# Performance work log

Hardware: AMD Instinct MI355X
Metric: run time of the kernel (lower is better)

Reference implementation:

```python
import jax, jax.numpy as jnp
import numpy as np

N_NODES = 100000
N_EDGES = 1600000
IN_DIM = 128      # 1 (degree) + 127 (raw feat)
HID = 128
N_GRAPHS = 100


def setup_inputs() -> dict:
    key = jax.random.key(0)
    ks = jax.random.split(key, 16)
    feat = jax.random.normal(ks[0], (N_NODES, IN_DIM - 1), dtype=jnp.float32)
    src = jax.random.randint(ks[1], (N_EDGES,), 0, N_NODES, dtype=jnp.int32)
    dst = jax.random.randint(ks[2], (N_EDGES,), 0, N_NODES, dtype=jnp.int32)
    graph_ids = jnp.sort(jax.random.randint(ks[3], (N_NODES,), 0, N_GRAPHS, dtype=jnp.int32))
    s = 1.0 / np.sqrt(IN_DIM)
    W0 = jax.random.uniform(ks[4], (HID, IN_DIM), jnp.float32, -s, s)
    b0 = jax.random.uniform(ks[5], (HID,), jnp.float32, -s, s)
    s = 1.0 / np.sqrt(HID)
    W1 = jax.random.uniform(ks[6], (HID, HID), jnp.float32, -s, s)
    b1 = jax.random.uniform(ks[7], (HID,), jnp.float32, -s, s)
    W2 = jax.random.uniform(ks[8], (HID, HID), jnp.float32, -s, s)
    b2 = jax.random.uniform(ks[9], (HID,), jnp.float32, -s, s)
    Wc1 = jax.random.uniform(ks[10], (HID, HID), jnp.float32, -s, s)
    bc1 = jax.random.uniform(ks[11], (HID,), jnp.float32, -s, s)
    Wc2 = jax.random.uniform(ks[12], (1, HID), jnp.float32, -s, s)
    bc2 = jax.random.uniform(ks[13], (1,), jnp.float32, -s, s)
    return {"feat": feat, "src": src, "dst": dst, "graph_ids": graph_ids,
            "num_graphs": N_GRAPHS,
            "W0": W0, "b0": b0, "W1": W1, "b1": b1, "W2": W2, "b2": b2,
            "Wc1": Wc1, "bc1": bc1, "Wc2": Wc2, "bc2": bc2}


def _gcn_layer(h, src, dst, deg, W, b):
    # mean over in-neighbor messages; zero-in-degree nodes keep old h (DGL reduce never fires)
    n = h.shape[0]
    summed = jax.ops.segment_sum(h[src], dst, num_segments=n)  # [N, d]
    mean = summed / jnp.maximum(deg, 1.0)[:, None]
    agg = jnp.where((deg > 0)[:, None], mean, h)
    return jax.nn.relu(agg @ W.T + b)


def reference(feat, src, dst, graph_ids, num_graphs,
              W0, b0, W1, b1, W2, b2, Wc1, bc1, Wc2, bc2):
    n = feat.shape[0]
    deg = jax.ops.segment_sum(jnp.ones(src.shape[0], jnp.float32), dst, num_segments=n)  # in-degrees
    h = jnp.concatenate([deg[:, None], feat], axis=-1)  # [N, IN_DIM]
    for W, b in ((W0, b0), (W1, b1), (W2, b2)):
        h = _gcn_layer(h, src, dst, deg, W, b)
    # dgl.mean_nodes: per-graph mean of node features
    counts = jax.ops.segment_sum(jnp.ones(n, jnp.float32), graph_ids, num_segments=num_graphs)
    hg = jax.ops.segment_sum(h, graph_ids, num_segments=num_graphs) / jnp.maximum(counts, 1.0)[:, None]
    # faithful: classify1 applied twice, no activation (F.relu was passed as bias flag)
    hg = hg @ Wc1.T + bc1
    hg = hg @ Wc1.T + bc1
    hg = hg @ Wc2.T + bc2
    return hg  # [num_graphs, 1]
```

## Files before the change

kernel.cpp:

```cpp
#include <hip/hip_runtime.h>
#include <hip/hip_bf16.h>

#define HID 128
#define NRAW 127
#define BSH 8
#define BNODES 256
#define EW 1536


typedef __attribute__((ext_vector_type(8))) short short8;
typedef __attribute__((ext_vector_type(4))) float floatx4;
typedef __attribute__((ext_vector_type(2))) float floatx2;

__device__ inline unsigned pack_bf2(float x, float y) {
    unsigned bx = __float_as_uint(x);
    unsigned by = __float_as_uint(y);
    bx += 0x7fffu + ((bx >> 16) & 1u);
    by += 0x7fffu + ((by >> 16) & 1u);
    return (bx >> 16) | (by & 0xffff0000u);
}
__device__ inline float bf_lo(unsigned u) { return __uint_as_float(u << 16); }
__device__ inline float bf_hi(unsigned u) { return __uint_as_float(u & 0xffff0000u); }


__global__ void init_kernel(const float* __restrict__ W0, const float* __restrict__ W1,
                            const float* __restrict__ W2, const float* __restrict__ Wc1,
                            unsigned* __restrict__ O0, unsigned* __restrict__ O1,
                            unsigned* __restrict__ O2, float* __restrict__ Wc1p,
                            int* __restrict__ gbucket, float* __restrict__ hg,
                            float* __restrict__ counts, int G) {
    int id = blockIdx.x * blockDim.x + threadIdx.x;
    if (id < 512) gbucket[id] = 0;
    if (id < G * HID) hg[id] = 0.f;
    if (id < G) counts[id] = 0.f;
    if (id < 16384) {
        int t = id >> 7, p = id & 127;
        Wc1p[id] = Wc1[t * 128 + ((p & 7) * 16 + (p >> 3))];
    }
    if (id < 3 * 8192) {
        int sel = id >> 13, l = id & 8191;
        const float* W = sel == 0 ? W0 : (sel == 1 ? W1 : W2);
        unsigned* O = sel == 0 ? O0 : (sel == 1 ? O1 : O2);
        int o = l >> 6, pp = (l & 63) * 2;
        int k0 = (pp & 7) * 16 + (pp >> 3);
        int k1 = ((pp + 1) & 7) * 16 + ((pp + 1) >> 3);
        O[l] = pack_bf2(W[o * 128 + k0], W[o * 128 + k1]);
    }
}


__global__ __launch_bounds__(256) void bucket_count_kernel(const int* __restrict__ dst,
                                                           int* __restrict__ gbucket,
                                                           int E, int NB) {
    __shared__ int hist[512];
    int t = threadIdx.x;
    for (int b = t; b < NB; b += 256) hist[b] = 0;
    __syncthreads();
    int base = blockIdx.x * 4096;
    #pragma unroll
    for (int j = 0; j < 16; ++j) {
        int e = base + j * 256 + t;
        if (e < E) atomicAdd(&hist[dst[e] >> BSH], 1);
    }
    __syncthreads();
    for (int b = t; b < NB; b += 256) {
        int v = hist[b];
        if (v) atomicAdd(&gbucket[b], v);
    }
}

__global__ void bucket_scan_kernel(const int* __restrict__ gbucket, int* __restrict__ bstart,
                                   int* __restrict__ gcur, int NB, int E) {
    __shared__ int sm[512];
    int t = threadIdx.x;
    int v = (t < NB) ? gbucket[t] : 0;
    sm[t] = v;
    __syncthreads();
    for (int off = 1; off < 512; off <<= 1) {
        int add = (t >= off) ? sm[t - off] : 0;
        __syncthreads();
        sm[t] += add;
        __syncthreads();
    }
    if (t < NB) {
        int ex = sm[t] - v;
        bstart[t] = ex;
        gcur[t] = ex;
    }
    if (t == 0) bstart[NB] = E;
}

__global__ __launch_bounds__(256) void bucket_scatter_kernel(const int* __restrict__ src,
                                                             const int* __restrict__ dst,
                                                             int* __restrict__ gcur,
                                                             unsigned* __restrict__ staging,
                                                             int E, int NB) {
    __shared__ int hist[512];
    __shared__ int base[512];
    int t = threadIdx.x;
    for (int b = t; b < NB; b += 256) hist[b] = 0;
    __syncthreads();
    int s[16], d[16], r[16];
    int e0 = blockIdx.x * 4096;
    #pragma unroll
    for (int j = 0; j < 16; ++j) {
        int e = e0 + j * 256 + t;
        if (e < E) {
            s[j] = src[e];
            d[j] = dst[e];
            r[j] = atomicAdd(&hist[d[j] >> BSH], 1);
        } else d[j] = -1;
    }
    __syncthreads();
    for (int b = t; b < NB; b += 256) {
        int v = hist[b];
        base[b] = v ? atomicAdd(&gcur[b], v) : 0;
    }
    __syncthreads();
    #pragma unroll
    for (int j = 0; j < 16; ++j) {
        if (d[j] >= 0) {
            int b = d[j] >> BSH;
            staging[base[b] + r[j]] = ((unsigned)s[j] << 8) | ((unsigned)d[j] & 255u);
        }
    }
}

__global__ __launch_bounds__(256) void csr_build_kernel(const unsigned* __restrict__ staging,
                                                        const int* __restrict__ bstart,
                                                        int* __restrict__ rp, int* __restrict__ csr,
                                                        float* __restrict__ degf,
                                                        int N, int E, int NB) {
    __shared__ int hist[256];
    __shared__ int sm[256];
    __shared__ int excl[256];
    __shared__ int cnt[256];
    int t = threadIdx.x;
    int b = blockIdx.x;
    int nbase = b << BSH;
    int s0 = bstart[b], e1 = bstart[b + 1];
    hist[t] = 0;
    __syncthreads();
    for (int i = s0 + t; i < e1; i += 256) {
        unsigned p = staging[i];
        atomicAdd(&hist[p & (BNODES - 1)], 1);
    }
    __syncthreads();
    int h = hist[t];
    sm[t] = h;
    __syncthreads();
    for (int off = 1; off < 256; off <<= 1) {
        int add = (t >= off) ? sm[t - off] : 0;
        __syncthreads();
        sm[t] += add;
        __syncthreads();
    }
    excl[t] = sm[t] - h;
    cnt[t] = 0;
    int n = nbase + t;
    if (n < N) {
        rp[n] = s0 + (sm[t] - h);
        degf[n] = (float)h;
    }
    if (b == NB - 1 && t == 0) rp[N] = E;
    __syncthreads();
    for (int i = s0 + t; i < e1; i += 256) {
        unsigned p = staging[i];
        int dl = p & (BNODES - 1);
        int pos = s0 + excl[dl] + atomicAdd(&cnt[dl], 1);
        csr[pos] = (int)(p >> 8);
    }
}


__global__ void build_h0_kernel(const float* __restrict__ feat,
                                unsigned* __restrict__ h8, int N) {
    int id = blockIdx.x * blockDim.x + threadIdx.x;
    if (id >= N * 32) return;
    int n = id >> 5, c = id & 31;
    const float* fr = feat + (size_t)n * NRAW;
    int base = c >> 1, hb = (c & 1) * 4;
    float f[4];
    #pragma unroll
    for (int j = 0; j < 4; ++j) {
        int l = (hb + j) * 16 + base;
        f[j] = (l == 0) ? 0.f : fr[l - 1];
    }
    unsigned w = __builtin_amdgcn_cvt_pk_fp8_f32(f[0], f[1], 0, false);
    w = __builtin_amdgcn_cvt_pk_fp8_f32(f[2], f[3], w, true);
    h8[id] = w;
}


__global__ __launch_bounds__(256) void gcn_fused_kernel(const unsigned* __restrict__ h8,
                                                        unsigned* __restrict__ out8,
                                                        unsigned* __restrict__ outb,
                                                        const unsigned* __restrict__ Wb,
                                                        const float* __restrict__ bias,
                                                        const int* __restrict__ rp,
                                                        const int* __restrict__ csr,
                                                        const float* __restrict__ degf, int N) {
    __shared__ unsigned Al[16 * 64];
    __shared__ unsigned Cs[16 * 64];
    __shared__ int sIdx[EW];
    int t = threadIdx.x;
    int col = t & 15;
    int g = t >> 4;
    int n0 = blockIdx.x * 16;
    int i = n0 + g;
    const char* hbase = (const char*)h8;
    unsigned cOff = (unsigned)col * 8u;

    int start = 0, end = 0;
    if (i < N) { start = rp[i]; end = rp[i + 1]; }
    int deg = end - start;
    int nEnd = min(n0 + 16, N);
    int s0 = rp[n0];
    int e1 = rp[nEnd];

    floatx2 a0 = {0.f, 0.f}, a1 = {0.f, 0.f}, a2 = {0.f, 0.f}, a3 = {0.f, 0.f};
    float dsum = 0.f;

    #define GATH(ii) (*(const uint2*)(hbase + (((unsigned)(ii) << 7) + cOff)))
    #define ACC(vv) do { \
        a0 += __builtin_amdgcn_cvt_pk_f32_fp8((vv).x, false); \
        a1 += __builtin_amdgcn_cvt_pk_f32_fp8((vv).x, true);  \
        a2 += __builtin_amdgcn_cvt_pk_f32_fp8((vv).y, false); \
        a3 += __builtin_amdgcn_cvt_pk_f32_fp8((vv).y, true);  \
    } while (0)

    for (int w0 = s0; w0 < e1; w0 += EW) {
        if (w0 > s0) __syncthreads();
        int wcnt = min(EW, e1 - w0);
        for (int j = t; j < wcnt; j += 256) sIdx[j] = csr[w0 + j];
        __syncthreads();
        int p = max(start, w0) - w0;
        int pe = min(end, w0 + wcnt) - w0;
        for (; p + 8 <= pe; p += 8) {
            int i0 = sIdx[p],     i1 = sIdx[p + 1], i2 = sIdx[p + 2], i3 = sIdx[p + 3];
            int i4 = sIdx[p + 4], i5 = sIdx[p + 5], i6 = sIdx[p + 6], i7 = sIdx[p + 7];
            uint2 v0 = GATH(i0), v1 = GATH(i1), v2 = GATH(i2), v3 = GATH(i3);
            uint2 v4 = GATH(i4), v5 = GATH(i5), v6 = GATH(i6), v7 = GATH(i7);
            if (degf && col == 0)
                dsum += degf[i0] + degf[i1] + degf[i2] + degf[i3]
                      + degf[i4] + degf[i5] + degf[i6] + degf[i7];
            ACC(v0); ACC(v1); ACC(v2); ACC(v3);
            ACC(v4); ACC(v5); ACC(v6); ACC(v7);
        }
        for (; p + 4 <= pe; p += 4) {
            int i0 = sIdx[p], i1 = sIdx[p + 1], i2 = sIdx[p + 2], i3 = sIdx[p + 3];
            uint2 v0 = GATH(i0), v1 = GATH(i1), v2 = GATH(i2), v3 = GATH(i3);
            if (degf && col == 0)
                dsum += degf[i0] + degf[i1] + degf[i2] + degf[i3];
            ACC(v0); ACC(v1); ACC(v2); ACC(v3);
        }
        for (; p < pe; ++p) {
            int i0 = sIdx[p];
            uint2 v0 = GATH(i0);
            if (degf && col == 0) dsum += degf[i0];
            ACC(v0);
        }
    }

    if (i < N) {
        uint4 r;
        if (deg == 0) {
            uint2 v = GATH(i);
            floatx2 l0 = __builtin_amdgcn_cvt_pk_f32_fp8(v.x, false);
            floatx2 h0 = __builtin_amdgcn_cvt_pk_f32_fp8(v.x, true);
            floatx2 l1 = __builtin_amdgcn_cvt_pk_f32_fp8(v.y, false);
            floatx2 h1 = __builtin_amdgcn_cvt_pk_f32_fp8(v.y, true);
            r.x = pack_bf2(l0[0], l0[1]);
            r.y = pack_bf2(h0[0], h0[1]);
            r.z = pack_bf2(l1[0], l1[1]);
            r.w = pack_bf2(h1[0], h1[1]);
        } else {
            if (degf && col == 0) a0[0] = dsum;
            float inv = 1.f / (float)deg;
            r.x = pack_bf2(a0[0] * inv, a0[1] * inv);
            r.y = pack_bf2(a1[0] * inv, a1[1] * inv);
            r.z = pack_bf2(a2[0] * inv, a2[1] * inv);
            r.w = pack_bf2(a3[0] * inv, a3[1] * inv);
        }
        *(uint4*)&Al[(g * 16 + (col ^ (g & 7))) * 4] = r;
    }
    __syncthreads();

    int wv = t >> 6, lane = t & 63;
    int m = lane & 15, q = lane >> 4;
    floatx4 acc0 = (floatx4)(0.f), acc1 = (floatx4)(0.f);
    #pragma unroll
    for (int kt = 0; kt < 4; ++kt) {
        short8 af = *(const short8*)&Al[(m * 16 + ((kt * 4 + q) ^ (m & 7))) * 4];
        short8 b0 = *(const short8*)&Wb[((2 * wv) * 16 + m) * 64 + kt * 16 + q * 4];
        short8 b1 = *(const short8*)&Wb[((2 * wv + 1) * 16 + m) * 64 + kt * 16 + q * 4];
        acc0 = __builtin_amdgcn_mfma_f32_16x16x32_bf16(af, b0, acc0, 0, 0, 0);
        acc1 = __builtin_amdgcn_mfma_f32_16x16x32_bf16(af, b1, acc1, 0, 0, 0);
    }
    float bv0 = bias[(2 * wv) * 16 + m];
    float bv1 = bias[(2 * wv + 1) * 16 + m];
    #pragma unroll
    for (int r4 = 0; r4 < 4; ++r4) {
        int row = q * 4 + r4;
        float v0 = fmaxf(acc0[r4] + bv0, 0.f);
        float v1 = fmaxf(acc1[r4] + bv1, 0.f);
        if (out8) {
            unsigned pk = __builtin_amdgcn_cvt_pk_fp8_f32(v0, v1, 0, false);
            *(unsigned short*)((char*)Cs + row * 128 + m * 8 + 2 * wv) = (unsigned short)pk;
        } else {
            Cs[row * 64 + m * 4 + wv] = pack_bf2(v0, v1);
        }
    }
    __syncthreads();

    {
        int row = t >> 4, c = t & 15;
        int n = n0 + row;
        if (n < N) {
            if (out8)
                ((uint2*)out8)[(size_t)n * 16 + c] =
                    *(const uint2*)((const char*)Cs + row * 128 + c * 8);
            else
                ((uint4*)outb)[(size_t)n * 16 + c] = *(const uint4*)&Cs[row * 64 + c * 4];
        }
    }
    #undef GATH
    #undef ACC
}


__global__ __launch_bounds__(256) void pool_kernel(const unsigned* __restrict__ h,
                                                   const int* __restrict__ gid,
                                                   float* __restrict__ hg,
                                                   float* __restrict__ counts, int N) {
    int c = threadIdx.x & 63;
    int q = threadIdx.x >> 6;
    int n0 = blockIdx.x * 64;
    int nend = min(n0 + 64, N);
    float ax = 0.f, ay = 0.f, cnt = 0.f;
    int cur = -1;
    for (int n = n0 + q; n < nend; n += 4) {
        int g = gid[n];
        if (g != cur) {
            if (cur >= 0) {
                atomicAdd(&hg[cur * HID + 2 * c], ax);
                atomicAdd(&hg[cur * HID + 2 * c + 1], ay);
                if (c == 0) atomicAdd(&counts[cur], cnt);
            }
            ax = ay = cnt = 0.f;
            cur = g;
        }
        unsigned v = h[(size_t)n * 64 + c];
        ax += bf_lo(v); ay += bf_hi(v);
        cnt += 1.f;
    }
    if (cur >= 0) {
        atomicAdd(&hg[cur * HID + 2 * c], ax);
        atomicAdd(&hg[cur * HID + 2 * c + 1], ay);
        if (c == 0) atomicAdd(&counts[cur], cnt);
    }
}


__global__ __launch_bounds__(128) void cls_fused_kernel(const float* __restrict__ hg,
                                                        const float* __restrict__ counts,
                                                        const float* __restrict__ Wc1p,
                                                        const float* __restrict__ Wc1,
                                                        const float* __restrict__ bc1,
                                                        const float* __restrict__ Wc2,
                                                        const float* __restrict__ bc2,
                                                        float* __restrict__ out, int G) {
    __shared__ float x[128];
    __shared__ float y[128];
    __shared__ float red[128];
    int g = blockIdx.x, t = threadIdx.x;
    float inv = 1.f / fmaxf(counts[g], 1.f);
    x[t] = hg[g * HID + t] * inv;
    __syncthreads();
    const float4* wp4 = (const float4*)(Wc1p + t * HID);
    float s = 0.f;
    #pragma unroll
    for (int k4 = 0; k4 < 32; ++k4) {
        float4 w = wp4[k4];
        s += x[k4 * 4] * w.x + x[k4 * 4 + 1] * w.y + x[k4 * 4 + 2] * w.z + x[k4 * 4 + 3] * w.w;
    }
    y[t] = s + bc1[t];
    __syncthreads();
    const float4* w4 = (const float4*)(Wc1 + t * HID);
    float s2 = 0.f;
    #pragma unroll
    for (int k4 = 0; k4 < 32; ++k4) {
        float4 w = w4[k4];
        s2 += y[k4 * 4] * w.x + y[k4 * 4 + 1] * w.y + y[k4 * 4 + 2] * w.z + y[k4 * 4 + 3] * w.w;
    }
    red[t] = (s2 + bc1[t]) * Wc2[t];
    __syncthreads();
    if (t < 64) {
        float r = red[t] + red[t + 64];
        #pragma unroll
        for (int off = 32; off > 0; off >>= 1) r += __shfl_down(r, off);
        if (t == 0) out[g] = r + bc2[0];
    }
}


extern "C" void kernel_launch(void* const* d_in, const int* in_sizes, int n_in,
                              void* d_out, int out_size, void* d_ws, size_t ws_size,
                              hipStream_t stream) {
    const float* feat = (const float*)d_in[0];
    const int* src    = (const int*)d_in[1];
    const int* dst    = (const int*)d_in[2];
    const int* gid    = (const int*)d_in[3];
    const float* W0  = (const float*)d_in[5];
    const float* b0  = (const float*)d_in[6];
    const float* W1  = (const float*)d_in[7];
    const float* b1  = (const float*)d_in[8];
    const float* W2  = (const float*)d_in[9];
    const float* b2  = (const float*)d_in[10];
    const float* Wc1 = (const float*)d_in[11];
    const float* bc1 = (const float*)d_in[12];
    const float* Wc2 = (const float*)d_in[13];
    const float* bc2 = (const float*)d_in[14];

    const int N = in_sizes[3];
    const int E = in_sizes[1];
    const int G = out_size;
    const int NB = (N + BNODES - 1) >> BSH;

    char* ws = (char*)d_ws;
    size_t off = 0;
    auto alloc = [&](size_t bytes) { void* p = ws + off; off += (bytes + 255) & ~size_t(255); return p; };
    unsigned* h8a    = (unsigned*)alloc((size_t)N * 32 * 4);
    unsigned* h8b    = (unsigned*)alloc((size_t)N * 32 * 4);
    unsigned* hB     = (unsigned*)alloc((size_t)N * 64 * 4);
    float* degf      = (float*)alloc((size_t)N * 4);
    unsigned* staging = (unsigned*)alloc((size_t)E * 4);
    int* csr         = (int*)alloc((size_t)E * 4);
    int* rp          = (int*)alloc((size_t)(N + 1) * 4);
    int* gbucket     = (int*)alloc(512 * 4);
    int* bstart      = (int*)alloc(513 * 4);
    int* gcur        = (int*)alloc(512 * 4);
    unsigned* Wb0    = (unsigned*)alloc(8192 * 4);
    unsigned* Wb1    = (unsigned*)alloc(8192 * 4);
    unsigned* Wb2    = (unsigned*)alloc(8192 * 4);
    float* Wc1p      = (float*)alloc(16384 * 4);
    float* hg        = (float*)alloc((size_t)G * HID * 4);
    float* counts    = (float*)alloc((size_t)G * 4);

    init_kernel<<<96, 256, 0, stream>>>(W0, W1, W2, Wc1, Wb0, Wb1, Wb2, Wc1p,
                                        gbucket, hg, counts, G);

    int gE = (E + 4095) / 4096;
    bucket_count_kernel<<<gE, 256, 0, stream>>>(dst, gbucket, E, NB);
    bucket_scan_kernel<<<1, 512, 0, stream>>>(gbucket, bstart, gcur, NB, E);
    bucket_scatter_kernel<<<gE, 256, 0, stream>>>(src, dst, gcur, staging, E, NB);
    csr_build_kernel<<<NB, 256, 0, stream>>>(staging, bstart, rp, csr, degf, N, E, NB);

    build_h0_kernel<<<(N * 32 + 255) / 256, 256, 0, stream>>>(feat, h8a, N);

    int layer_grid = (N + 15) / 16;
    gcn_fused_kernel<<<layer_grid, 256, 0, stream>>>(h8a, h8b, nullptr, Wb0, b0, rp, csr, degf, N);
    gcn_fused_kernel<<<layer_grid, 256, 0, stream>>>(h8b, h8a, nullptr, Wb1, b1, rp, csr, nullptr, N);
    gcn_fused_kernel<<<layer_grid, 256, 0, stream>>>(h8a, nullptr, hB, Wb2, b2, rp, csr, nullptr, N);

    pool_kernel<<<(N + 63) / 64, 256, 0, stream>>>(hB, gid, hg, counts, N);

    cls_fused_kernel<<<G, 128, 0, stream>>>(hg, counts, Wc1p, Wc1, bc1, Wc2, bc2,
                                            (float*)d_out, G);
}
```

Before: 361.5 us.

## Pad CSR rows to multiples of eight and software-pipeline neighbor gathers

```diff
diff --git a/kernel.cpp b/kernel.cpp
--- a/kernel.cpp
+++ b/kernel.cpp
@@ -28,11 +28,17 @@
                             unsigned* __restrict__ O0, unsigned* __restrict__ O1,
                             unsigned* __restrict__ O2, float* __restrict__ Wc1p,
                             int* __restrict__ gbucket, float* __restrict__ hg,
-                            float* __restrict__ counts, int G) {
+                            float* __restrict__ counts,
+                            unsigned* __restrict__ h8a, unsigned* __restrict__ h8b,
+                            int G, int N) {
     int id = blockIdx.x * blockDim.x + threadIdx.x;
     if (id < 512) gbucket[id] = 0;
     if (id < G * HID) hg[id] = 0.f;
     if (id < G) counts[id] = 0.f;
+    if (id < 32) {
+        h8a[(size_t)N * 32 + id] = 0u;
+        h8b[(size_t)N * 32 + id] = 0u;
+    }
     if (id < 16384) {
         int t = id >> 7, p = id & 127;
         Wc1p[id] = Wc1[t * 128 + ((p & 7) * 16 + (p >> 3))];
@@ -147,7 +153,8 @@
     }
     __syncthreads();
     int h = hist[t];
-    sm[t] = h;
+    int hp = h ? (h + 7) & ~7 : 0;
+    sm[t] = hp;
     __syncthreads();
     for (int off = 1; off < 256; off <<= 1) {
         int add = (t >= off) ? sm[t - off] : 0;
@@ -155,21 +162,27 @@
         sm[t] += add;
         __syncthreads();
     }
-    excl[t] = sm[t] - h;
+    int ex = sm[t] - hp;
+    excl[t] = ex;
     cnt[t] = 0;
+    int pb = ((s0 + 7) & ~7) + b * 2048;
     int n = nbase + t;
     if (n < N) {
-        rp[n] = s0 + (sm[t] - h);
+        rp[n] = pb + ex;
         degf[n] = (float)h;
     }
-    if (b == NB - 1 && t == 0) rp[N] = E;
+    if (b == NB - 1 && t == 255) {
+        rp[N] = pb + sm[255];
+        degf[N] = 0.f;
+    }
     __syncthreads();
     for (int i = s0 + t; i < e1; i += 256) {
         unsigned p = staging[i];
         int dl = p & (BNODES - 1);
-        int pos = s0 + excl[dl] + atomicAdd(&cnt[dl], 1);
+        int pos = pb + excl[dl] + atomicAdd(&cnt[dl], 1);
         csr[pos] = (int)(p >> 8);
     }
+    for (int j = h; j < hp; ++j) csr[pb + ex + j] = N;
 }
 
 
@@ -192,17 +205,18 @@
 }
 
 
-__global__ __launch_bounds__(256) void gcn_fused_kernel(const unsigned* __restrict__ h8,
-                                                        unsigned* __restrict__ out8,
-                                                        unsigned* __restrict__ outb,
-                                                        const unsigned* __restrict__ Wb,
-                                                        const float* __restrict__ bias,
-                                                        const int* __restrict__ rp,
-                                                        const int* __restrict__ csr,
-                                                        const float* __restrict__ degf, int N) {
+__global__ __launch_bounds__(256, 4) void gcn_fused_kernel(const unsigned* __restrict__ h8,
+                                                           unsigned* __restrict__ out8,
+                                                           unsigned* __restrict__ outb,
+                                                           const unsigned* __restrict__ Wb,
+                                                           const float* __restrict__ bias,
+                                                           const int* __restrict__ rp,
+                                                           const int* __restrict__ csr,
+                                                           const float* __restrict__ degf,
+                                                           int col0fix, int N) {
     __shared__ unsigned Al[16 * 64];
     __shared__ unsigned Cs[16 * 64];
-    __shared__ int sIdx[EW];
+    __shared__ __align__(16) int sIdx[EW];
     int t = threadIdx.x;
     int col = t & 15;
     int g = t >> 4;
@@ -211,12 +225,16 @@
     const char* hbase = (const char*)h8;
     unsigned cOff = (unsigned)col * 8u;
 
-    int start = 0, end = 0;
-    if (i < N) { start = rp[i]; end = rp[i + 1]; }
-    int deg = end - start;
+    int deg = 0, start = 0, end = 0;
+    if (i < N) {
+        start = rp[i];
+        deg = (int)degf[i];
+        end = start + ((deg + 7) & ~7);
+    }
     int nEnd = min(n0 + 16, N);
     int s0 = rp[n0];
-    int e1 = rp[nEnd];
+    int lastd = (int)degf[nEnd - 1];
+    int e1 = rp[nEnd - 1] + ((lastd + 7) & ~7);
 
     floatx2 a0 = {0.f, 0.f}, a1 = {0.f, 0.f}, a2 = {0.f, 0.f}, a3 = {0.f, 0.f};
     float dsum = 0.f;
@@ -228,37 +246,54 @@
         a2 += __builtin_amdgcn_cvt_pk_f32_fp8((vv).y, false); \
         a3 += __builtin_amdgcn_cvt_pk_f32_fp8((vv).y, true);  \
     } while (0)
+    #define LOADC(V, pp) do { \
+        int4 _ja = *(const int4*)&sIdx[(pp)]; \
+        int4 _jb = *(const int4*)&sIdx[(pp) + 4]; \
+        V##0 = GATH(_ja.x); V##1 = GATH(_ja.y); V##2 = GATH(_ja.z); V##3 = GATH(_ja.w); \
+        V##4 = GATH(_jb.x); V##5 = GATH(_jb.y); V##6 = GATH(_jb.z); V##7 = GATH(_jb.w); \
+    } while (0)
+    #define ACCC(V, pp) do { \
+        if (col0fix && col == 0) { \
+            dsum += degf[sIdx[(pp)]] + degf[sIdx[(pp) + 1]] + degf[sIdx[(pp) + 2]] \
+                  + degf[sIdx[(pp) + 3]] + degf[sIdx[(pp) + 4]] + degf[sIdx[(pp) + 5]] \
+                  + degf[sIdx[(pp) + 6]] + degf[sIdx[(pp) + 7]]; \
+        } \
+        ACC(V##0); ACC(V##1); ACC(V##2); ACC(V##3); \
+        ACC(V##4); ACC(V##5); ACC(V##6); ACC(V##7); \
+    } while (0)
+
+    uint2 A0, A1, A2, A3, A4, A5, A6, A7;
+    uint2 B0, B1, B2, B3, B4, B5, B6, B7;
 
     for (int w0 = s0; w0 < e1; w0 += EW) {
         if (w0 > s0) __syncthreads();
         int wcnt = min(EW, e1 - w0);
-        for (int j = t; j < wcnt; j += 256) sIdx[j] = csr[w0 + j];
+        for (int j = t * 4; j < wcnt; j += 1024)
+            *(int4*)&sIdx[j] = *(const int4*)&csr[w0 + j];
         __syncthreads();
-        int p = max(start, w0) - w0;
+        int p  = max(start, w0) - w0;
         int pe = min(end, w0 + wcnt) - w0;
-        for (; p + 8 <= pe; p += 8) {
-            int i0 = sIdx[p],     i1 = sIdx[p + 1], i2 = sIdx[p + 2], i3 = sIdx[p + 3];
-            int i4 = sIdx[p + 4], i5 = sIdx[p + 5], i6 = sIdx[p + 6], i7 = sIdx[p + 7];
-            uint2 v0 = GATH(i0), v1 = GATH(i1), v2 = GATH(i2), v3 = GATH(i3);
-            uint2 v4 = GATH(i4), v5 = GATH(i5), v6 = GATH(i6), v7 = GATH(i7);
-            if (degf && col == 0)
-                dsum += degf[i0] + degf[i1] + degf[i2] + degf[i3]
-                      + degf[i4] + degf[i5] + degf[i6] + degf[i7];
-            ACC(v0); ACC(v1); ACC(v2); ACC(v3);
-            ACC(v4); ACC(v5); ACC(v6); ACC(v7);
-        }
-        for (; p + 4 <= pe; p += 4) {
-            int i0 = sIdx[p], i1 = sIdx[p + 1], i2 = sIdx[p + 2], i3 = sIdx[p + 3];
-            uint2 v0 = GATH(i0), v1 = GATH(i1), v2 = GATH(i2), v3 = GATH(i3);
-            if (degf && col == 0)
-                dsum += degf[i0] + degf[i1] + degf[i2] + degf[i3];
-            ACC(v0); ACC(v1); ACC(v2); ACC(v3);
-        }
-        for (; p < pe; ++p) {
-            int i0 = sIdx[p];
-            uint2 v0 = GATH(i0);
-            if (degf && col == 0) dsum += degf[i0];
-            ACC(v0);
+        if (p < pe) {
+            int pA = p;
+            LOADC(A, pA);
+            p += 8;
+            while (p + 16 <= pe) {
+                int pB = p;
+                LOADC(B, pB);
+                ACCC(A, pA);
+                pA = p + 8;
+                LOADC(A, pA);
+                ACCC(B, pB);
+                p += 16;
+            }
+            if (p < pe) {
+                int pB = p;
+                LOADC(B, pB);
+                ACCC(A, pA);
+                ACCC(B, pB);
+            } else {
+                ACCC(A, pA);
+            }
         }
     }
 
@@ -275,7 +310,7 @@
             r.z = pack_bf2(l1[0], l1[1]);
             r.w = pack_bf2(h1[0], h1[1]);
         } else {
-            if (degf && col == 0) a0[0] = dsum;
+            if (col0fix && col == 0) a0[0] = dsum;
             float inv = 1.f / (float)deg;
             r.x = pack_bf2(a0[0] * inv, a0[1] * inv);
             r.y = pack_bf2(a1[0] * inv, a1[1] * inv);
@@ -326,6 +361,8 @@
     }
     #undef GATH
     #undef ACC
+    #undef LOADC
+    #undef ACCC
 }
 
 
@@ -430,12 +467,12 @@
     char* ws = (char*)d_ws;
     size_t off = 0;
     auto alloc = [&](size_t bytes) { void* p = ws + off; off += (bytes + 255) & ~size_t(255); return p; };
-    unsigned* h8a    = (unsigned*)alloc((size_t)N * 32 * 4);
-    unsigned* h8b    = (unsigned*)alloc((size_t)N * 32 * 4);
+    unsigned* h8a    = (unsigned*)alloc((size_t)(N + 1) * 32 * 4);
+    unsigned* h8b    = (unsigned*)alloc((size_t)(N + 1) * 32 * 4);
     unsigned* hB     = (unsigned*)alloc((size_t)N * 64 * 4);
-    float* degf      = (float*)alloc((size_t)N * 4);
+    float* degf      = (float*)alloc((size_t)(N + 1) * 4);
     unsigned* staging = (unsigned*)alloc((size_t)E * 4);
-    int* csr         = (int*)alloc((size_t)E * 4);
+    int* csr         = (int*)alloc((size_t)(E + (NB + 1) * 2048 + 64) * 4);
     int* rp          = (int*)alloc((size_t)(N + 1) * 4);
     int* gbucket     = (int*)alloc(512 * 4);
     int* bstart      = (int*)alloc(513 * 4);
@@ -448,7 +485,7 @@
     float* counts    = (float*)alloc((size_t)G * 4);
 
     init_kernel<<<96, 256, 0, stream>>>(W0, W1, W2, Wc1, Wb0, Wb1, Wb2, Wc1p,
-                                        gbucket, hg, counts, G);
+                                        gbucket, hg, counts, h8a, h8b, G, N);
 
     int gE = (E + 4095) / 4096;
     bucket_count_kernel<<<gE, 256, 0, stream>>>(dst, gbucket, E, NB);
@@ -459,9 +496,9 @@
     build_h0_kernel<<<(N * 32 + 255) / 256, 256, 0, stream>>>(feat, h8a, N);
 
     int layer_grid = (N + 15) / 16;
-    gcn_fused_kernel<<<layer_grid, 256, 0, stream>>>(h8a, h8b, nullptr, Wb0, b0, rp, csr, degf, N);
-    gcn_fused_kernel<<<layer_grid, 256, 0, stream>>>(h8b, h8a, nullptr, Wb1, b1, rp, csr, nullptr, N);
-    gcn_fused_kernel<<<layer_grid, 256, 0, stream>>>(h8a, nullptr, hB, Wb2, b2, rp, csr, nullptr, N);
+    gcn_fused_kernel<<<layer_grid, 256, 0, stream>>>(h8a, h8b, nullptr, Wb0, b0, rp, csr, degf, 1, N);
+    gcn_fused_kernel<<<layer_grid, 256, 0, stream>>>(h8b, h8a, nullptr, Wb1, b1, rp, csr, degf, 0, N);
+    gcn_fused_kernel<<<layer_grid, 256, 0, stream>>>(h8a, nullptr, hB, Wb2, b2, rp, csr, degf, 0, N);
 
     pool_kernel<<<(N + 63) / 64, 256, 0, stream>>>(hB, gid, hg, counts, N);
 
```

Result: slower. 385.1 us (+6.5%).

## Split each node's neighbor gather across four lane groups and coalesce h0 build

Applied to the files above, without the earlier changes.

```diff
diff --git a/kernel.cpp b/kernel.cpp
--- a/kernel.cpp
+++ b/kernel.cpp
@@ -5,7 +5,6 @@
 #define NRAW 127
 #define BSH 8
 #define BNODES 256
-#define EW 1536
 
 
 typedef __attribute__((ext_vector_type(8))) short short8;
@@ -28,11 +27,17 @@
                             unsigned* __restrict__ O0, unsigned* __restrict__ O1,
                             unsigned* __restrict__ O2, float* __restrict__ Wc1p,
                             int* __restrict__ gbucket, float* __restrict__ hg,
-                            float* __restrict__ counts, int G) {
+                            float* __restrict__ counts,
+                            unsigned* __restrict__ h8a, unsigned* __restrict__ h8b,
+                            int G, int N) {
     int id = blockIdx.x * blockDim.x + threadIdx.x;
     if (id < 512) gbucket[id] = 0;
     if (id < G * HID) hg[id] = 0.f;
     if (id < G) counts[id] = 0.f;
+    if (id < 32) {
+        h8a[(size_t)N * 32 + id] = 0u;
+        h8b[(size_t)N * 32 + id] = 0u;
+    }
     if (id < 16384) {
         int t = id >> 7, p = id & 127;
         Wc1p[id] = Wc1[t * 128 + ((p & 7) * 16 + (p >> 3))];
@@ -162,7 +167,10 @@
         rp[n] = s0 + (sm[t] - h);
         degf[n] = (float)h;
     }
-    if (b == NB - 1 && t == 0) rp[N] = E;
+    if (b == NB - 1 && t == 0) {
+        rp[N] = E;
+        degf[N] = 0.f;
+    }
     __syncthreads();
     for (int i = s0 + t; i < e1; i += 256) {
         unsigned p = staging[i];
@@ -173,22 +181,29 @@
 }
 
 
-__global__ void build_h0_kernel(const float* __restrict__ feat,
-                                unsigned* __restrict__ h8, int N) {
-    int id = blockIdx.x * blockDim.x + threadIdx.x;
-    if (id >= N * 32) return;
-    int n = id >> 5, c = id & 31;
-    const float* fr = feat + (size_t)n * NRAW;
-    int base = c >> 1, hb = (c & 1) * 4;
-    float f[4];
-    #pragma unroll
-    for (int j = 0; j < 4; ++j) {
-        int l = (hb + j) * 16 + base;
-        f[j] = (l == 0) ? 0.f : fr[l - 1];
-    }
-    unsigned w = __builtin_amdgcn_cvt_pk_fp8_f32(f[0], f[1], 0, false);
-    w = __builtin_amdgcn_cvt_pk_fp8_f32(f[2], f[3], w, true);
-    h8[id] = w;
+__global__ __launch_bounds__(256) void build_h0_kernel(const float* __restrict__ feat,
+                                                       unsigned* __restrict__ h8, int N) {
+    __shared__ float lf[8 * NRAW];
+    int t = threadIdx.x;
+    int n0 = blockIdx.x * 8;
+    int nrows = min(8, N - n0);
+    int total = nrows * NRAW;
+    for (int j = t; j < total; j += 256) lf[j] = feat[(size_t)n0 * NRAW + j];
+    __syncthreads();
+    int n = t >> 5, c = t & 31;
+    if (n < nrows) {
+        const float* fr = lf + n * NRAW;
+        int base = c >> 1, hb = (c & 1) * 4;
+        float f[4];
+        #pragma unroll
+        for (int j = 0; j < 4; ++j) {
+            int l = (hb + j) * 16 + base;
+            f[j] = (l == 0) ? 0.f : fr[l - 1];
+        }
+        unsigned w = __builtin_amdgcn_cvt_pk_fp8_f32(f[0], f[1], 0, false);
+        w = __builtin_amdgcn_cvt_pk_fp8_f32(f[2], f[3], w, true);
+        h8[(size_t)(n0 + n) * 32 + c] = w;
+    }
 }
 
 
@@ -199,133 +214,126 @@
                                                         const float* __restrict__ bias,
                                                         const int* __restrict__ rp,
                                                         const int* __restrict__ csr,
-                                                        const float* __restrict__ degf, int N) {
+                                                        const float* __restrict__ degf,
+                                                        int col0fix, int N) {
     __shared__ unsigned Al[16 * 64];
     __shared__ unsigned Cs[16 * 64];
-    __shared__ int sIdx[EW];
-    int t = threadIdx.x;
-    int col = t & 15;
-    int g = t >> 4;
+    int t = threadIdx.x;
+    int wv = t >> 6, lane = t & 63;
+    int s = lane >> 4;
+    int c = lane & 15;
     int n0 = blockIdx.x * 16;
-    int i = n0 + g;
     const char* hbase = (const char*)h8;
-    unsigned cOff = (unsigned)col * 8u;
-
-    int start = 0, end = 0;
-    if (i < N) { start = rp[i]; end = rp[i + 1]; }
-    int deg = end - start;
-    int nEnd = min(n0 + 16, N);
-    int s0 = rp[n0];
-    int e1 = rp[nEnd];
-
-    floatx2 a0 = {0.f, 0.f}, a1 = {0.f, 0.f}, a2 = {0.f, 0.f}, a3 = {0.f, 0.f};
-    float dsum = 0.f;
-
-    #define GATH(ii) (*(const uint2*)(hbase + (((unsigned)(ii) << 7) + cOff)))
-    #define ACC(vv) do { \
-        a0 += __builtin_amdgcn_cvt_pk_f32_fp8((vv).x, false); \
-        a1 += __builtin_amdgcn_cvt_pk_f32_fp8((vv).x, true);  \
-        a2 += __builtin_amdgcn_cvt_pk_f32_fp8((vv).y, false); \
-        a3 += __builtin_amdgcn_cvt_pk_f32_fp8((vv).y, true);  \
-    } while (0)
-
-    for (int w0 = s0; w0 < e1; w0 += EW) {
-        if (w0 > s0) __syncthreads();
-        int wcnt = min(EW, e1 - w0);
-        for (int j = t; j < wcnt; j += 256) sIdx[j] = csr[w0 + j];
-        __syncthreads();
-        int p = max(start, w0) - w0;
-        int pe = min(end, w0 + wcnt) - w0;
-        for (; p + 8 <= pe; p += 8) {
-            int i0 = sIdx[p],     i1 = sIdx[p + 1], i2 = sIdx[p + 2], i3 = sIdx[p + 3];
-            int i4 = sIdx[p + 4], i5 = sIdx[p + 5], i6 = sIdx[p + 6], i7 = sIdx[p + 7];
-            uint2 v0 = GATH(i0), v1 = GATH(i1), v2 = GATH(i2), v3 = GATH(i3);
-            uint2 v4 = GATH(i4), v5 = GATH(i5), v6 = GATH(i6), v7 = GATH(i7);
-            if (degf && col == 0)
-                dsum += degf[i0] + degf[i1] + degf[i2] + degf[i3]
-                      + degf[i4] + degf[i5] + degf[i6] + degf[i7];
-            ACC(v0); ACC(v1); ACC(v2); ACC(v3);
-            ACC(v4); ACC(v5); ACC(v6); ACC(v7);
-        }
-        for (; p + 4 <= pe; p += 4) {
-            int i0 = sIdx[p], i1 = sIdx[p + 1], i2 = sIdx[p + 2], i3 = sIdx[p + 3];
-            uint2 v0 = GATH(i0), v1 = GATH(i1), v2 = GATH(i2), v3 = GATH(i3);
-            if (degf && col == 0)
-                dsum += degf[i0] + degf[i1] + degf[i2] + degf[i3];
-            ACC(v0); ACC(v1); ACC(v2); ACC(v3);
-        }
-        for (; p < pe; ++p) {
-            int i0 = sIdx[p];
-            uint2 v0 = GATH(i0);
-            if (degf && col == 0) dsum += degf[i0];
-            ACC(v0);
-        }
-    }
-
-    if (i < N) {
-        uint4 r;
-        if (deg == 0) {
-            uint2 v = GATH(i);
+    unsigned cOff = (unsigned)c * 8u;
+
+    for (int nn = 0; nn < 4; ++nn) {
+        int g = wv * 4 + nn;
+        int i = n0 + g;
+        if (i >= N) break;
+        int start = rp[i], end = rp[i + 1];
+        int deg = end - start;
+        floatx2 a0 = {0.f, 0.f}, a1 = {0.f, 0.f}, a2 = {0.f, 0.f}, a3 = {0.f, 0.f};
+        float dsum = 0.f;
+
+        if (deg > 0) {
+            int q = start + s;
+            int idx = N;
+            if (q < end) idx = csr[q];
+            for (int p = start; p < end; p += 4) {
+                uint2 v = *(const uint2*)(hbase + (((unsigned)idx << 7) + cOff));
+                float dg = 0.f;
+                if (col0fix && c == 0) dg = degf[idx];
+                int q2 = p + 4 + s;
+                int idxN = N;
+                if (q2 < end) idxN = csr[q2];
+                a0 += __builtin_amdgcn_cvt_pk_f32_fp8(v.x, false);
+                a1 += __builtin_amdgcn_cvt_pk_f32_fp8(v.x, true);
+                a2 += __builtin_amdgcn_cvt_pk_f32_fp8(v.y, false);
+                a3 += __builtin_amdgcn_cvt_pk_f32_fp8(v.y, true);
+                if (col0fix && c == 0) dsum += dg;
+                idx = idxN;
+            }
+            a0[0] += __shfl_xor(a0[0], 16); a0[1] += __shfl_xor(a0[1], 16);
+            a1[0] += __shfl_xor(a1[0], 16); a1[1] += __shfl_xor(a1[1], 16);
+            a2[0] += __shfl_xor(a2[0], 16); a2[1] += __shfl_xor(a2[1], 16);
+            a3[0] += __shfl_xor(a3[0], 16); a3[1] += __shfl_xor(a3[1], 16);
+            a0[0] += __shfl_xor(a0[0], 32); a0[1] += __shfl_xor(a0[1], 32);
+            a1[0] += __shfl_xor(a1[0], 32); a1[1] += __shfl_xor(a1[1], 32);
+            a2[0] += __shfl_xor(a2[0], 32); a2[1] += __shfl_xor(a2[1], 32);
+            a3[0] += __shfl_xor(a3[0], 32); a3[1] += __shfl_xor(a3[1], 32);
+            if (col0fix) {
+                dsum += __shfl_xor(dsum, 16);
+                dsum += __shfl_xor(dsum, 32);
+            }
+        }
+
+        float f0, f1, f2, f3, f4, f5, f6, f7;
+        if (deg > 0) {
+            if (col0fix && c == 0) a0[0] = dsum;
+            float inv = 1.f / (float)deg;
+            f0 = a0[0] * inv; f1 = a0[1] * inv;
+            f2 = a1[0] * inv; f3 = a1[1] * inv;
+            f4 = a2[0] * inv; f5 = a2[1] * inv;
+            f6 = a3[0] * inv; f7 = a3[1] * inv;
+        } else {
+            uint2 v = *(const uint2*)(hbase + (((unsigned)i << 7) + cOff));
             floatx2 l0 = __builtin_amdgcn_cvt_pk_f32_fp8(v.x, false);
             floatx2 h0 = __builtin_amdgcn_cvt_pk_f32_fp8(v.x, true);
             floatx2 l1 = __builtin_amdgcn_cvt_pk_f32_fp8(v.y, false);
             floatx2 h1 = __builtin_amdgcn_cvt_pk_f32_fp8(v.y, true);
-            r.x = pack_bf2(l0[0], l0[1]);
-            r.y = pack_bf2(h0[0], h0[1]);
-            r.z = pack_bf2(l1[0], l1[1]);
-            r.w = pack_bf2(h1[0], h1[1]);
-        } else {
-            if (degf && col == 0) a0[0] = dsum;
-            float inv = 1.f / (float)deg;
-            r.x = pack_bf2(a0[0] * inv, a0[1] * inv);
-            r.y = pack_bf2(a1[0] * inv, a1[1] * inv);
-            r.z = pack_bf2(a2[0] * inv, a2[1] * inv);
-            r.w = pack_bf2(a3[0] * inv, a3[1] * inv);
-        }
-        *(uint4*)&Al[(g * 16 + (col ^ (g & 7))) * 4] = r;
-    }
-    __syncthreads();
-
-    int wv = t >> 6, lane = t & 63;
-    int m = lane & 15, q = lane >> 4;
-    floatx4 acc0 = (floatx4)(0.f), acc1 = (floatx4)(0.f);
-    #pragma unroll
-    for (int kt = 0; kt < 4; ++kt) {
-        short8 af = *(const short8*)&Al[(m * 16 + ((kt * 4 + q) ^ (m & 7))) * 4];
-        short8 b0 = *(const short8*)&Wb[((2 * wv) * 16 + m) * 64 + kt * 16 + q * 4];
-        short8 b1 = *(const short8*)&Wb[((2 * wv + 1) * 16 + m) * 64 + kt * 16 + q * 4];
-        acc0 = __builtin_amdgcn_mfma_f32_16x16x32_bf16(af, b0, acc0, 0, 0, 0);
-        acc1 = __builtin_amdgcn_mfma_f32_16x16x32_bf16(af, b1, acc1, 0, 0, 0);
-    }
-    float bv0 = bias[(2 * wv) * 16 + m];
-    float bv1 = bias[(2 * wv + 1) * 16 + m];
-    #pragma unroll
-    for (int r4 = 0; r4 < 4; ++r4) {
-        int row = q * 4 + r4;
-        float v0 = fmaxf(acc0[r4] + bv0, 0.f);
-        float v1 = fmaxf(acc1[r4] + bv1, 0.f);
-        if (out8) {
-            unsigned pk = __builtin_amdgcn_cvt_pk_fp8_f32(v0, v1, 0, false);
-            *(unsigned short*)((char*)Cs + row * 128 + m * 8 + 2 * wv) = (unsigned short)pk;
-        } else {
-            Cs[row * 64 + m * 4 + wv] = pack_bf2(v0, v1);
+            f0 = l0[0]; f1 = l0[1]; f2 = h0[0]; f3 = h0[1];
+            f4 = l1[0]; f5 = l1[1]; f6 = h1[0]; f7 = h1[1];
+        }
+        if (s == 0) {
+            uint4 r;
+            r.x = pack_bf2(f0, f1);
+            r.y = pack_bf2(f2, f3);
+            r.z = pack_bf2(f4, f5);
+            r.w = pack_bf2(f6, f7);
+            *(uint4*)&Al[(g * 16 + (c ^ (g & 7))) * 4] = r;
         }
     }
     __syncthreads();
 
     {
-        int row = t >> 4, c = t & 15;
+        int m = lane & 15, q = lane >> 4;
+        floatx4 acc0 = (floatx4)(0.f), acc1 = (floatx4)(0.f);
+        #pragma unroll
+        for (int kt = 0; kt < 4; ++kt) {
+            short8 af = *(const short8*)&Al[(m * 16 + ((kt * 4 + q) ^ (m & 7))) * 4];
+            short8 b0 = *(const short8*)&Wb[((2 * wv) * 16 + m) * 64 + kt * 16 + q * 4];
+            short8 b1 = *(const short8*)&Wb[((2 * wv + 1) * 16 + m) * 64 + kt * 16 + q * 4];
+            acc0 = __builtin_amdgcn_mfma_f32_16x16x32_bf16(af, b0, acc0, 0, 0, 0);
+            acc1 = __builtin_amdgcn_mfma_f32_16x16x32_bf16(af, b1, acc1, 0, 0, 0);
+        }
+        float bv0 = bias[(2 * wv) * 16 + m];
+        float bv1 = bias[(2 * wv + 1) * 16 + m];
+        #pragma unroll
+        for (int r4 = 0; r4 < 4; ++r4) {
+            int row = q * 4 + r4;
+            float v0 = fmaxf(acc0[r4] + bv0, 0.f);
+            float v1 = fmaxf(acc1[r4] + bv1, 0.f);
+            if (out8) {
+                unsigned pk = __builtin_amdgcn_cvt_pk_fp8_f32(v0, v1, 0, false);
+                *(unsigned short*)((char*)Cs + row * 128 + m * 8 + 2 * wv) = (unsigned short)pk;
+            } else {
+                Cs[row * 64 + m * 4 + wv] = pack_bf2(v0, v1);
+            }
+        }
+    }
+    __syncthreads();
+
+    {
+        int row = t >> 4, cc = t & 15;
         int n = n0 + row;
         if (n < N) {
             if (out8)
-                ((uint2*)out8)[(size_t)n * 16 + c] =
-                    *(const uint2*)((const char*)Cs + row * 128 + c * 8);
+                ((uint2*)out8)[(size_t)n * 16 + cc] =
+                    *(const uint2*)((const char*)Cs + row * 128 + cc * 8);
             else
-                ((uint4*)outb)[(size_t)n * 16 + c] = *(const uint4*)&Cs[row * 64 + c * 4];
-        }
-    }
-    #undef GATH
-    #undef ACC
+                ((uint4*)outb)[(size_t)n * 16 + cc] = *(const uint4*)&Cs[row * 64 + cc * 4];
+        }
+    }
 }
 
 
@@ -430,12 +438,12 @@
     char* ws = (char*)d_ws;
     size_t off = 0;
     auto alloc = [&](size_t bytes) { void* p = ws + off; off += (bytes + 255) & ~size_t(255); return p; };
-    unsigned* h8a    = (unsigned*)alloc((size_t)N * 32 * 4);
-    unsigned* h8b    = (unsigned*)alloc((size_t)N * 32 * 4);
+    unsigned* h8a    = (unsigned*)alloc((size_t)(N + 1) * 32 * 4);
+    unsigned* h8b    = (unsigned*)alloc((size_t)(N + 1) * 32 * 4);
     unsigned* hB     = (unsigned*)alloc((size_t)N * 64 * 4);
-    float* degf      = (float*)alloc((size_t)N * 4);
+    float* degf      = (float*)alloc((size_t)(N + 1) * 4);
     unsigned* staging = (unsigned*)alloc((size_t)E * 4);
-    int* csr         = (int*)alloc((size_t)E * 4);
+    int* csr         = (int*)alloc((size_t)(E + 64) * 4);
     int* rp          = (int*)alloc((size_t)(N + 1) * 4);
     int* gbucket     = (int*)alloc(512 * 4);
     int* bstart      = (int*)alloc(513 * 4);
@@ -448,7 +456,7 @@
     float* counts    = (float*)alloc((size_t)G * 4);
 
     init_kernel<<<96, 256, 0, stream>>>(W0, W1, W2, Wc1, Wb0, Wb1, Wb2, Wc1p,
-                                        gbucket, hg, counts, G);
+                                        gbucket, hg, counts, h8a, h8b, G, N);
 
     int gE = (E + 4095) / 4096;
     bucket_count_kernel<<<gE, 256, 0, stream>>>(dst, gbucket, E, NB);
@@ -456,12 +464,12 @@
     bucket_scatter_kernel<<<gE, 256, 0, stream>>>(src, dst, gcur, staging, E, NB);
     csr_build_kernel<<<NB, 256, 0, stream>>>(staging, bstart, rp, csr, degf, N, E, NB);
 
-    build_h0_kernel<<<(N * 32 + 255) / 256, 256, 0, stream>>>(feat, h8a, N);
+    build_h0_kernel<<<(N + 7) / 8, 256, 0, stream>>>(feat, h8a, N);
 
     int layer_grid = (N + 15) / 16;
-    gcn_fused_kernel<<<layer_grid, 256, 0, stream>>>(h8a, h8b, nullptr, Wb0, b0, rp, csr, degf, N);
-    gcn_fused_kernel<<<layer_grid, 256, 0, stream>>>(h8b, h8a, nullptr, Wb1, b1, rp, csr, nullptr, N);
-    gcn_fused_kernel<<<layer_grid, 256, 0, stream>>>(h8a, nullptr, hB, Wb2, b2, rp, csr, nullptr, N);
+    gcn_fused_kernel<<<layer_grid, 256, 0, stream>>>(h8a, h8b, nullptr, Wb0, b0, rp, csr, degf, 1, N);
+    gcn_fused_kernel<<<layer_grid, 256, 0, stream>>>(h8b, h8a, nullptr, Wb1, b1, rp, csr, degf, 0, N);
+    gcn_fused_kernel<<<layer_grid, 256, 0, stream>>>(h8a, nullptr, hB, Wb2, b2, rp, csr, degf, 0, N);
 
     pool_kernel<<<(N + 63) / 64, 256, 0, stream>>>(hB, gid, hg, counts, N);
 
```

Result: slower. 421.8 us (+16.7%).
